# Performance work log

Measured on AMD Instinct MI355X. Metric: run time of the kernel, lower is better.

## Reference

```python
import jax, jax.numpy as jnp
import numpy as np

N_MB, H, K = 4, 8, 64
C = N_MB * N_MB + 1  # 17 edge types (incl. padding type 0)
B, S = 8, 512


def setup_inputs() -> dict:
    key = jax.random.key(0)
    k1, k2, k3, k4, k5 = jax.random.split(key, 5)
    p_attn = jax.random.uniform(k1, (B, H, S, S), dtype=jnp.float32)
    value = jax.random.normal(k2, (B, H, S, K), dtype=jnp.float32)
    b_seq = jax.random.randint(k3, (B, S), 0, N_MB + 1, dtype=jnp.int32)
    W2 = jax.random.normal(k4, (N_MB, H, K, K), dtype=jnp.float32) * 0.02
    alpha2 = jax.random.normal(k5, (C, N_MB, H), dtype=jnp.float32) * 0.02
    return {"p_attn": p_attn, "value": value, "b_seq": b_seq, "W2": W2, "alpha2": alpha2}


def reference(p_attn, value, b_seq, W2, alpha2):
    n_mb = W2.shape[0]
    n_types = n_mb * n_mb + 1
    # Pairwise edge-type matrix: 0 if either endpoint is padding (b_seq==0),
    # else (b_i - 1) * n_mb + b_j in [1, n_mb^2].
    bi = b_seq[:, :, None]
    bj = b_seq[:, None, :]
    b_mat = ((bi - 1) * n_mb + bj) * (bi * bj != 0).astype(jnp.int32)  # (b,i,j)
    # Mixture-of-behaviors value transform per (edge-type, head).
    W2_ = jnp.einsum('BhdD,CBh->ChdD', W2, jax.nn.softmax(alpha2, axis=1))  # (C,h,k,k)
    # Equivalent to the one-hot einsum, but never materializes (b,h,i,j,C):
    # out[b,h,i,D] = sum_c sum_j p_attn * [b_mat==c] * value @ W2_[c]
    out = jnp.zeros(p_attn.shape[:3] + (value.shape[-1],), dtype=value.dtype)
    for c in range(n_types):  # small fixed loop over edge types
        mask_c = (b_mat == c).astype(p_attn.dtype)  # (b,i,j)
        tmp = jnp.einsum('bhij,bij,bhjd->bhid', p_attn, mask_c, value)
        out = out + jnp.einsum('bhid,hdD->bhiD', tmp, W2_[c])
    return out
```

## Files before the change

### kernel.cpp

```cpp
#include <hip/hip_runtime.h>
#include <hip/hip_bf16.h>
#include <stdint.h>

#define B_ 8
#define H_ 8
#define S_ 512
#define K_ 64
#define NMB_ 4
#define NG_ 5

typedef unsigned short u16;
typedef __attribute__((ext_vector_type(8))) short short8;
typedef __attribute__((ext_vector_type(4))) float f32x4;

#define OFF_PERM 0
#define OFF_WST  16384

#define VT_STRIDE 520
#define VT_U16    (64 * VT_STRIDE)
#define MP_U16    (320 * 8)

__device__ __forceinline__ u16 f2b(float f) {
    __hip_bfloat16 h = __float2bfloat16(f);
    return *reinterpret_cast<u16*>(&h);
}
__device__ __forceinline__ int clamp5(int g) {
    g = g < 0 ? 0 : g;
    return g > (NG_ - 1) ? (NG_ - 1) : g;
}
__device__ __forceinline__ short8 and8(short8 a, short8 m) {
    int4 x = *reinterpret_cast<int4*>(&a);
    int4 y = *reinterpret_cast<int4*>(&m);
    int4 r = make_int4(x.x & y.x, x.y & y.y, x.z & y.z, x.w & y.w);
    return *reinterpret_cast<short8*>(&r);
}

__global__ void k_sort(const int* __restrict__ b_seq, int* __restrict__ perm) {
    const int b = blockIdx.x;
    const int lane = threadIdx.x;
    const int* bs = b_seq + b * S_;

    int tot[NG_] = {0,0,0,0,0};
    for (int ch = 0; ch < S_ / 64; ++ch) {
        int g = clamp5(bs[ch * 64 + lane]);
        for (int bin = 0; bin < NG_; ++bin) {
            unsigned long long m = __ballot(g == bin);
            tot[bin] += (int)__popcll(m);
        }
    }
    int starts[NG_]; int run = 0;
    for (int bin = 0; bin < NG_; ++bin) { starts[bin] = run; run += tot[bin]; }

    int running[NG_] = {0,0,0,0,0};
    unsigned long long lt = (1ull << lane) - 1ull;
    for (int ch = 0; ch < S_ / 64; ++ch) {
        int i = ch * 64 + lane;
        int g = clamp5(bs[i]);
        int pos = 0;
        for (int bin = 0; bin < NG_; ++bin) {
            unsigned long long m = __ballot(g == bin);
            if (g == bin) pos = starts[bin] + running[bin] + (int)__popcll(m & lt);
            running[bin] += (int)__popcll(m);
        }
        perm[b * S_ + pos] = i;
    }
}

__global__ void k_w2s(const float* __restrict__ W2, const float* __restrict__ al,
                      u16* __restrict__ Wst) {
    const int h = blockIdx.x / NG_, bi = blockIdx.x % NG_;
    float sm[NG_][NMB_];
#pragma unroll
    for (int g = 0; g < NG_; ++g) {
        int c = (bi == 0 || g == 0) ? 0 : (bi - 1) * NMB_ + g;
        float a[NMB_]; float mx = -1e30f;
#pragma unroll
        for (int m = 0; m < NMB_; ++m) { a[m] = al[(c * NMB_ + m) * H_ + h]; mx = fmaxf(mx, a[m]); }
        float s = 0.f;
#pragma unroll
        for (int m = 0; m < NMB_; ++m) { a[m] = __expf(a[m] - mx); s += a[m]; }
        float inv = 1.f / s;
#pragma unroll
        for (int m = 0; m < NMB_; ++m) sm[g][m] = a[m] * inv;
    }
    for (int e = threadIdx.x; e < 320 * 64; e += 256) {
        int k = e >> 6, D = e & 63;
        int g = k >> 6, d = k & 63;
        float acc = 0.f;
#pragma unroll
        for (int m = 0; m < NMB_; ++m)
            acc += sm[g][m] * W2[((m * H_ + h) * K_ + d) * K_ + D];
        int kt = k >> 5, kk = k & 31;
        Wst[(((h * NG_ + bi) * 10 + kt) * 64 + D) * 32 + kk] = f2b(acc);
    }
}

__global__ __launch_bounds__(256) void k_main(const float* __restrict__ P,
                                              const float* __restrict__ V,
                                              const int* __restrict__ b_seq,
                                              const int* __restrict__ perm,
                                              const u16* __restrict__ Wst,
                                              float* __restrict__ out) {
    __shared__ __align__(16) u16 smem[VT_U16 + MP_U16];
    u16* vT = smem;
    u16* mp = smem + VT_U16;
    const int b = blockIdx.z, h = blockIdx.y;
    const int w = threadIdx.y;
    const int lane = threadIdx.x;
    const int tid = w * 64 + lane;
    const int r16 = lane & 15, quad = lane >> 4;
    const int tile = blockIdx.x * 4 + w;
    const int bh = b * H_ + h;

    const float* vsrc = V + (size_t)bh * S_ * K_;
#pragma unroll
    for (int c = 0; c < 32; ++c) {
        int e = c * 1024 + tid * 4;
        int j = e >> 6, d = e & 63;
        float4 v = *reinterpret_cast<const float4*>(vsrc + e);
        vT[(d + 0) * VT_STRIDE + j] = f2b(v.x);
        vT[(d + 1) * VT_STRIDE + j] = f2b(v.y);
        vT[(d + 2) * VT_STRIDE + j] = f2b(v.z);
        vT[(d + 3) * VT_STRIDE + j] = f2b(v.w);
    }
    for (int e = tid; e < 320; e += 256) {
        int kt = e / 20, rem = e % 20, g = rem >> 2, q = rem & 3;
        uint32_t dw[4];
#pragma unroll
        for (int t = 0; t < 4; ++t) {
            int k = kt * 32 + q * 8 + t * 2;
            uint32_t lo = (clamp5(b_seq[b * S_ + k])     == g) ? 0xFFFFu : 0u;
            uint32_t hi = (clamp5(b_seq[b * S_ + k + 1]) == g) ? 0xFFFF0000u : 0u;
            dw[t] = lo | hi;
        }
        *reinterpret_cast<uint4*>(mp + e * 8) = make_uint4(dw[0], dw[1], dw[2], dw[3]);
    }
    const int vi  = perm[b * S_ + tile * 16 + r16] & (S_ - 1);
    const int vbi = clamp5(b_seq[b * S_ + vi]);
    __syncthreads();

    f32x4 acc1[20];
#pragma unroll
    for (int nt = 0; nt < 20; ++nt) acc1[nt] = (f32x4){0.f, 0.f, 0.f, 0.f};

    const float* aP = P + ((size_t)bh * S_ + vi) * S_ + quad * 8;
    float4 ax = *reinterpret_cast<const float4*>(aP);
    float4 ay = *reinterpret_cast<const float4*>(aP + 4);
    for (int kt = 0; kt < 16; ++kt) {
        float4 axn, ayn;
        if (kt < 15) {
            axn = *reinterpret_cast<const float4*>(aP + (kt + 1) * 32);
            ayn = *reinterpret_cast<const float4*>(aP + (kt + 1) * 32 + 4);
        }
        short8 afrag;
        afrag[0] = (short)f2b(ax.x); afrag[1] = (short)f2b(ax.y);
        afrag[2] = (short)f2b(ax.z); afrag[3] = (short)f2b(ax.w);
        afrag[4] = (short)f2b(ay.x); afrag[5] = (short)f2b(ay.y);
        afrag[6] = (short)f2b(ay.z); afrag[7] = (short)f2b(ay.w);
        short8 vf[4];
#pragma unroll
        for (int dt = 0; dt < 4; ++dt)
            vf[dt] = *reinterpret_cast<const short8*>(
                &vT[(dt * 16 + r16) * VT_STRIDE + kt * 32 + quad * 8]);
#pragma unroll
        for (int g = 0; g < NG_; ++g) {
            short8 mk = *reinterpret_cast<const short8*>(mp + ((kt * 5 + g) * 4 + quad) * 8);
#pragma unroll
            for (int dt = 0; dt < 4; ++dt) {
                short8 bfrag = and8(vf[dt], mk);
                acc1[g * 4 + dt] =
                    __builtin_amdgcn_mfma_f32_16x16x32_bf16(afrag, bfrag, acc1[g * 4 + dt], 0, 0, 0);
            }
        }
        ax = axn; ay = ayn;
    }
    __syncthreads();

    u16* st = smem + w * (16 * 328);
#pragma unroll
    for (int nt = 0; nt < 20; ++nt)
#pragma unroll
        for (int r = 0; r < 4; ++r) {
            int row = quad * 4 + r;
            st[row * 328 + nt * 16 + r16] = f2b(acc1[nt][r]);
        }

    int blo = __shfl(vbi, 0), bhi = __shfl(vbi, 15);
    if (bhi < blo) bhi = blo;
    for (int blk = blo; blk <= bhi; ++blk) {
        f32x4 acc2[4];
#pragma unroll
        for (int nt = 0; nt < 4; ++nt) acc2[nt] = (f32x4){0.f, 0.f, 0.f, 0.f};
        const u16* wb = Wst + ((size_t)(h * NG_ + blk) * 10) * 2048 + r16 * 32 + quad * 8;
        for (int kt = 0; kt < 10; ++kt) {
            short8 a2 = *reinterpret_cast<const short8*>(&st[r16 * 328 + kt * 32 + quad * 8]);
#pragma unroll
            for (int nt = 0; nt < 4; ++nt) {
                short8 b2 = *reinterpret_cast<const short8*>(wb + kt * 2048 + nt * 512);
                acc2[nt] = __builtin_amdgcn_mfma_f32_16x16x32_bf16(a2, b2, acc2[nt], 0, 0, 0);
            }
        }
#pragma unroll
        for (int r = 0; r < 4; ++r) {
            int row = quad * 4 + r;
            int bir = __shfl(vbi, row);
            int ir  = __shfl(vi, row);
            if (bir == blk) {
#pragma unroll
                for (int nt = 0; nt < 4; ++nt)
                    out[((size_t)bh * S_ + ir) * K_ + nt * 16 + r16] = acc2[nt][r];
            }
        }
    }
}

extern "C" void kernel_launch(void* const* d_in, const int* in_sizes, int n_in,
                              void* d_out, int out_size, void* d_ws, size_t ws_size,
                              hipStream_t stream) {
    const float* p_attn = (const float*)d_in[0];
    const float* value  = (const float*)d_in[1];
    const int*   b_seq  = (const int*)d_in[2];
    const float* W2     = (const float*)d_in[3];
    const float* alpha2 = (const float*)d_in[4];

    char* ws = (char*)d_ws;
    int* perm = (int*)(ws + OFF_PERM);
    u16* Wst  = (u16*)(ws + OFF_WST);

    hipLaunchKernelGGL(k_sort, dim3(B_), dim3(64), 0, stream, b_seq, perm);
    hipLaunchKernelGGL(k_w2s, dim3(H_ * NG_), dim3(256), 0, stream, W2, alpha2, Wst);
    hipLaunchKernelGGL(k_main, dim3(8, H_, B_), dim3(64, 4), 0, stream,
                       p_attn, value, b_seq, perm, Wst, (float*)d_out);
}
```

Baseline: 160.1 us.

## Precompute bf16 fragment-ordered V in prep kernel and merge setup kernels

Merges the sort and W2-mixing kernels into one prep launch. That launch also converts V to bf16 once per (b,h) in MFMA-fragment order in global memory. The main kernel now streams V fragments directly from global/L2 instead of each of 8 blocks per (b,h) re-reading fp32 V and transposing it into LDS with scattered 2-byte writes. This cuts redundant conversion, LDS footprint and one sync. The cost is an extra workspace round trip and global loads inside the MFMA loop.

```diff
diff --git a/kernel.cpp b/kernel.cpp
--- a/kernel.cpp
+++ b/kernel.cpp
@@ -15,10 +15,10 @@
 
 #define OFF_PERM 0
 #define OFF_WST  16384
-
-#define VT_STRIDE 520
-#define VT_U16    (64 * VT_STRIDE)
-#define MP_U16    (320 * 8)
+#define OFF_VTF  1654784
+
+#define ST_U16 (4 * 16 * 328)
+#define MP_U16 (320 * 8)
 
 __device__ __forceinline__ u16 f2b(float f) {
     __hip_bfloat16 h = __float2bfloat16(f);
@@ -35,75 +35,117 @@
     return *reinterpret_cast<short8*>(&r);
 }
 
-__global__ void k_sort(const int* __restrict__ b_seq, int* __restrict__ perm) {
-    const int b = blockIdx.x;
-    const int lane = threadIdx.x;
-    const int* bs = b_seq + b * S_;
-
-    int tot[NG_] = {0,0,0,0,0};
-    for (int ch = 0; ch < S_ / 64; ++ch) {
-        int g = clamp5(bs[ch * 64 + lane]);
-        for (int bin = 0; bin < NG_; ++bin) {
-            unsigned long long m = __ballot(g == bin);
-            tot[bin] += (int)__popcll(m);
-        }
-    }
-    int starts[NG_]; int run = 0;
-    for (int bin = 0; bin < NG_; ++bin) { starts[bin] = run; run += tot[bin]; }
-
-    int running[NG_] = {0,0,0,0,0};
-    unsigned long long lt = (1ull << lane) - 1ull;
-    for (int ch = 0; ch < S_ / 64; ++ch) {
-        int i = ch * 64 + lane;
-        int g = clamp5(bs[i]);
-        int pos = 0;
-        for (int bin = 0; bin < NG_; ++bin) {
-            unsigned long long m = __ballot(g == bin);
-            if (g == bin) pos = starts[bin] + running[bin] + (int)__popcll(m & lt);
-            running[bin] += (int)__popcll(m);
-        }
-        perm[b * S_ + pos] = i;
-    }
-}
-
-__global__ void k_w2s(const float* __restrict__ W2, const float* __restrict__ al,
-                      u16* __restrict__ Wst) {
-    const int h = blockIdx.x / NG_, bi = blockIdx.x % NG_;
-    float sm[NG_][NMB_];
-#pragma unroll
-    for (int g = 0; g < NG_; ++g) {
-        int c = (bi == 0 || g == 0) ? 0 : (bi - 1) * NMB_ + g;
-        float a[NMB_]; float mx = -1e30f;
-#pragma unroll
-        for (int m = 0; m < NMB_; ++m) { a[m] = al[(c * NMB_ + m) * H_ + h]; mx = fmaxf(mx, a[m]); }
-        float s = 0.f;
-#pragma unroll
-        for (int m = 0; m < NMB_; ++m) { a[m] = __expf(a[m] - mx); s += a[m]; }
-        float inv = 1.f / s;
-#pragma unroll
-        for (int m = 0; m < NMB_; ++m) sm[g][m] = a[m] * inv;
-    }
-    for (int e = threadIdx.x; e < 320 * 64; e += 256) {
-        int k = e >> 6, D = e & 63;
-        int g = k >> 6, d = k & 63;
-        float acc = 0.f;
-#pragma unroll
-        for (int m = 0; m < NMB_; ++m)
-            acc += sm[g][m] * W2[((m * H_ + h) * K_ + d) * K_ + D];
-        int kt = k >> 5, kk = k & 31;
-        Wst[(((h * NG_ + bi) * 10 + kt) * 64 + D) * 32 + kk] = f2b(acc);
+__global__ __launch_bounds__(256) void k_prep(const float* __restrict__ V,
+                                              const int* __restrict__ b_seq,
+                                              const float* __restrict__ W2,
+                                              const float* __restrict__ al,
+                                              int* __restrict__ perm,
+                                              u16* __restrict__ Wst,
+                                              u16* __restrict__ vTf) {
+    __shared__ u16 vs[128 * 72];
+    const int bx = blockIdx.x;
+    const int tid = threadIdx.x;
+
+    if (bx < 8) {
+        if (tid >= 64) return;
+        const int b = bx, lane = tid;
+        const int* bs = b_seq + b * S_;
+        int tot[NG_] = {0,0,0,0,0};
+        for (int ch = 0; ch < S_ / 64; ++ch) {
+            int g = clamp5(bs[ch * 64 + lane]);
+            for (int bin = 0; bin < NG_; ++bin) {
+                unsigned long long m = __ballot(g == bin);
+                tot[bin] += (int)__popcll(m);
+            }
+        }
+        int starts[NG_]; int run = 0;
+        for (int bin = 0; bin < NG_; ++bin) { starts[bin] = run; run += tot[bin]; }
+        int running[NG_] = {0,0,0,0,0};
+        unsigned long long lt = (1ull << lane) - 1ull;
+        for (int ch = 0; ch < S_ / 64; ++ch) {
+            int i = ch * 64 + lane;
+            int g = clamp5(bs[i]);
+            int pos = 0;
+            for (int bin = 0; bin < NG_; ++bin) {
+                unsigned long long m = __ballot(g == bin);
+                if (g == bin) pos = starts[bin] + running[bin] + (int)__popcll(m & lt);
+                running[bin] += (int)__popcll(m);
+            }
+            perm[b * S_ + pos] = i;
+        }
+    } else if (bx < 48) {
+        const int h = (bx - 8) / NG_, bi = (bx - 8) % NG_;
+        float sm[NG_][NMB_];
+#pragma unroll
+        for (int g = 0; g < NG_; ++g) {
+            int c = (bi == 0 || g == 0) ? 0 : (bi - 1) * NMB_ + g;
+            float a[NMB_]; float mx = -1e30f;
+#pragma unroll
+            for (int m = 0; m < NMB_; ++m) { a[m] = al[(c * NMB_ + m) * H_ + h]; mx = fmaxf(mx, a[m]); }
+            float s = 0.f;
+#pragma unroll
+            for (int m = 0; m < NMB_; ++m) { a[m] = __expf(a[m] - mx); s += a[m]; }
+            float inv = 1.f / s;
+#pragma unroll
+            for (int m = 0; m < NMB_; ++m) sm[g][m] = a[m] * inv;
+        }
+        for (int e = tid; e < 320 * 64; e += 256) {
+            int k = e >> 6, D = e & 63;
+            int g = k >> 6, d = k & 63;
+            float acc = 0.f;
+#pragma unroll
+            for (int m = 0; m < NMB_; ++m)
+                acc += sm[g][m] * W2[((m * H_ + h) * K_ + d) * K_ + D];
+            int kt = k >> 5, kk = k & 31;
+            Wst[(((h * NG_ + bi) * 10 + kt) * 64 + D) * 32 + kk] = f2b(acc);
+        }
+    } else {
+        const int bh = bx - 48;
+        const float* vsrc = V + (size_t)bh * S_ * K_;
+        u16* dst = vTf + (size_t)bh * 32768;
+        for (int c = 0; c < 4; ++c) {
+#pragma unroll
+            for (int it = 0; it < 8; ++it) {
+                int f = (it * 256 + tid) * 4;
+                int jL = f >> 6, d = f & 63;
+                float4 v = *reinterpret_cast<const float4*>(vsrc + (size_t)(c * 128 + jL) * 64 + d);
+                uint2 pk;
+                pk.x = (uint32_t)f2b(v.x) | ((uint32_t)f2b(v.y) << 16);
+                pk.y = (uint32_t)f2b(v.z) | ((uint32_t)f2b(v.w) << 16);
+                *reinterpret_cast<uint2*>(&vs[jL * 72 + d]) = pk;
+            }
+            __syncthreads();
+#pragma unroll
+            for (int it = 0; it < 4; ++it) {
+                int idx = it * 256 + tid;
+                int quad = idx & 3, r = (idx >> 2) & 15, ktL = (idx >> 6) & 3, dt = idx >> 8;
+                int d = dt * 16 + r;
+                u16 o[8];
+#pragma unroll
+                for (int t = 0; t < 8; ++t)
+                    o[t] = vs[(ktL * 32 + quad * 8 + t) * 72 + d];
+                uint4 w;
+                w.x = (uint32_t)o[0] | ((uint32_t)o[1] << 16);
+                w.y = (uint32_t)o[2] | ((uint32_t)o[3] << 16);
+                w.z = (uint32_t)o[4] | ((uint32_t)o[5] << 16);
+                w.w = (uint32_t)o[6] | ((uint32_t)o[7] << 16);
+                int kt = c * 4 + ktL;
+                *reinterpret_cast<uint4*>(dst + (size_t)((dt * 16 + kt) * 16 + r) * 32 + quad * 8) = w;
+            }
+            __syncthreads();
+        }
     }
 }
 
 __global__ __launch_bounds__(256) void k_main(const float* __restrict__ P,
-                                              const float* __restrict__ V,
                                               const int* __restrict__ b_seq,
                                               const int* __restrict__ perm,
+                                              const u16* __restrict__ vTf,
                                               const u16* __restrict__ Wst,
                                               float* __restrict__ out) {
-    __shared__ __align__(16) u16 smem[VT_U16 + MP_U16];
-    u16* vT = smem;
-    u16* mp = smem + VT_U16;
+    __shared__ __align__(16) u16 smem[ST_U16 + MP_U16];
+    u16* st_all = smem;
+    u16* mp = smem + ST_U16;
     const int b = blockIdx.z, h = blockIdx.y;
     const int w = threadIdx.y;
     const int lane = threadIdx.x;
@@ -112,17 +154,6 @@
     const int tile = blockIdx.x * 4 + w;
     const int bh = b * H_ + h;
 
-    const float* vsrc = V + (size_t)bh * S_ * K_;
-#pragma unroll
-    for (int c = 0; c < 32; ++c) {
-        int e = c * 1024 + tid * 4;
-        int j = e >> 6, d = e & 63;
-        float4 v = *reinterpret_cast<const float4*>(vsrc + e);
-        vT[(d + 0) * VT_STRIDE + j] = f2b(v.x);
-        vT[(d + 1) * VT_STRIDE + j] = f2b(v.y);
-        vT[(d + 2) * VT_STRIDE + j] = f2b(v.z);
-        vT[(d + 3) * VT_STRIDE + j] = f2b(v.w);
-    }
     for (int e = tid; e < 320; e += 256) {
         int kt = e / 20, rem = e % 20, g = rem >> 2, q = rem & 3;
         uint32_t dw[4];
@@ -144,6 +175,7 @@
     for (int nt = 0; nt < 20; ++nt) acc1[nt] = (f32x4){0.f, 0.f, 0.f, 0.f};
 
     const float* aP = P + ((size_t)bh * S_ + vi) * S_ + quad * 8;
+    const u16* vb = vTf + (size_t)bh * 32768 + r16 * 32 + quad * 8;
     float4 ax = *reinterpret_cast<const float4*>(aP);
     float4 ay = *reinterpret_cast<const float4*>(aP + 4);
     for (int kt = 0; kt < 16; ++kt) {
@@ -152,16 +184,15 @@
             axn = *reinterpret_cast<const float4*>(aP + (kt + 1) * 32);
             ayn = *reinterpret_cast<const float4*>(aP + (kt + 1) * 32 + 4);
         }
+        short8 vf[4];
+#pragma unroll
+        for (int dt = 0; dt < 4; ++dt)
+            vf[dt] = *reinterpret_cast<const short8*>(vb + dt * 8192 + kt * 512);
         short8 afrag;
         afrag[0] = (short)f2b(ax.x); afrag[1] = (short)f2b(ax.y);
         afrag[2] = (short)f2b(ax.z); afrag[3] = (short)f2b(ax.w);
         afrag[4] = (short)f2b(ay.x); afrag[5] = (short)f2b(ay.y);
         afrag[6] = (short)f2b(ay.z); afrag[7] = (short)f2b(ay.w);
-        short8 vf[4];
-#pragma unroll
-        for (int dt = 0; dt < 4; ++dt)
-            vf[dt] = *reinterpret_cast<const short8*>(
-                &vT[(dt * 16 + r16) * VT_STRIDE + kt * 32 + quad * 8]);
 #pragma unroll
         for (int g = 0; g < NG_; ++g) {
             short8 mk = *reinterpret_cast<const short8*>(mp + ((kt * 5 + g) * 4 + quad) * 8);
@@ -174,9 +205,8 @@
         }
         ax = axn; ay = ayn;
     }
-    __syncthreads();
-
-    u16* st = smem + w * (16 * 328);
+
+    u16* st = st_all + w * (16 * 328);
 #pragma unroll
     for (int nt = 0; nt < 20; ++nt)
 #pragma unroll
@@ -226,9 +256,10 @@
     char* ws = (char*)d_ws;
     int* perm = (int*)(ws + OFF_PERM);
     u16* Wst  = (u16*)(ws + OFF_WST);
-
-    hipLaunchKernelGGL(k_sort, dim3(B_), dim3(64), 0, stream, b_seq, perm);
-    hipLaunchKernelGGL(k_w2s, dim3(H_ * NG_), dim3(256), 0, stream, W2, alpha2, Wst);
+    u16* vTf  = (u16*)(ws + OFF_VTF);
+
+    hipLaunchKernelGGL(k_prep, dim3(112), dim3(256), 0, stream,
+                       value, b_seq, W2, alpha2, perm, Wst, vTf);
     hipLaunchKernelGGL(k_main, dim3(8, H_, B_), dim3(64, 4), 0, stream,
-                       p_attn, value, b_seq, perm, Wst, (float*)d_out);
-}
+                       p_attn, b_seq, perm, vTf, Wst, (float*)d_out);
+}
```

New measurement: 152.3 us. -4.9%, faster.
